# Kernel optimization log

Measured on AMD Instinct MI355X. Metric: run time of the kernel, lower is better.

The kernel has to match this reference:

```python
import jax, jax.numpy as jnp
import numpy as np

N, E, D = 20000, 320000, 256
EPS = 1e-5


def setup_inputs() -> dict:
    key = jax.random.key(0)
    ks = jax.random.split(key, 12)
    s = 1.0 / np.sqrt(D)
    s2 = 1.0 / np.sqrt(2 * D)
    return {
        "node_embeddings": jax.random.normal(ks[0], (N, D), jnp.float32),
        "edge_index": jax.random.randint(ks[1], (2, E), 0, N, jnp.int64),
        "edge_embeddings": jax.random.normal(ks[2], (E, D), jnp.float32),
        # message MLP: Linear(D,D) -> GELU -> Linear(D,D)
        "W1m": jax.random.uniform(ks[3], (D, D), jnp.float32, -s, s),
        "b1m": jnp.zeros((D,), jnp.float32),
        "W2m": jax.random.uniform(ks[4], (D, D), jnp.float32, -s, s),
        "b2m": jnp.zeros((D,), jnp.float32),
        # update MLP: Linear(D,2D) -> GELU -> Linear(2D,D)
        "W1u": jax.random.uniform(ks[5], (D, 2 * D), jnp.float32, -s, s),
        "b1u": jnp.zeros((2 * D,), jnp.float32),
        "W2u": jax.random.uniform(ks[6], (2 * D, D), jnp.float32, -s2, s2),
        "b2u": jnp.zeros((D,), jnp.float32),
        # LayerNorm params
        "gamma": jnp.ones((D,), jnp.float32),
        "beta": jnp.zeros((D,), jnp.float32),
    }


def _layer_norm(x, gamma, beta):
    mu = jnp.mean(x, axis=-1, keepdims=True)
    var = jnp.mean(jnp.square(x - mu), axis=-1, keepdims=True)
    return (x - mu) * jax.lax.rsqrt(var + EPS) * gamma + beta


def reference(node_embeddings, edge_index, edge_embeddings,
              W1m, b1m, W2m, b2m, W1u, b1u, W2u, b2u, gamma, beta):
    src = edge_index[0]
    dst = edge_index[1]
    n = node_embeddings.shape[0]
    # gather + edge add + message MLP (exact erf GELU, as torch default)
    h = node_embeddings[src] + edge_embeddings           # [E, D]
    h = jax.nn.gelu(h @ W1m + b1m, approximate=False)
    messages = h @ W2m + b2m                             # [E, D]
    # scatter-mean aggregation
    agg = jax.ops.segment_sum(messages, dst, num_segments=n)  # [N, D]
    deg = jax.ops.segment_sum(jnp.ones((dst.shape[0], 1), node_embeddings.dtype),
                              dst, num_segments=n)            # [N, 1]
    agg = agg / jnp.maximum(deg, 1.0)
    # update MLP + residual + LayerNorm
    u = jax.nn.gelu(agg @ W1u + b1u, approximate=False) @ W2u + b2u
    return _layer_norm(node_embeddings + u, gamma, beta)
```

## Files before the change

kernel.cpp:

```cpp
#include <hip/hip_runtime.h>
#include <hip/hip_bf16.h>

#define N_NODES 20000
#define N_EDGES 320000
#define EBLK 64
#define NBLK 32

typedef __attribute__((ext_vector_type(8))) short short8;
typedef __attribute__((ext_vector_type(4))) float f32x4;

static __device__ __forceinline__ unsigned short f2bf(float f) {
  __hip_bfloat16 h = __float2bfloat16(f);
  union { __hip_bfloat16 h; unsigned short u; } cv; cv.h = h; return cv.u;
}

static __device__ __forceinline__ unsigned int pk2(float a, float b) {
  return (unsigned int)f2bf(a) | ((unsigned int)f2bf(b) << 16);
}

static __device__ __forceinline__ float gelu_f(float x) {
  float z = x * (2.3022082f + 0.1029432f * x * x);
  z = fminf(fmaxf(z, -30.0f), 30.0f);
  float t = exp2f(z);
  return x * t * __frcp_rn(1.0f + t);
}

#define SWZ(row, byteoff) ((byteoff) ^ (((row) & 7) << 4))
#define SWZU(b) ((b) ^ ((((b) >> 8) & 7) << 4))

__global__ void init_kernel(float4* __restrict__ S4, int4* __restrict__ cnt4,
                            const float* __restrict__ W1m, const float* __restrict__ W2m,
                            const float* __restrict__ W1u, const float* __restrict__ W2u,
                            unsigned short* __restrict__ P1m, unsigned short* __restrict__ P2m,
                            unsigned short* __restrict__ P1u, unsigned short* __restrict__ P2u) {
  const int b = blockIdx.x;
  if (b < 5000) {
    int idx = b * blockDim.x + threadIdx.x;
    S4[idx] = make_float4(0.f, 0.f, 0.f, 0.f);
    if (idx < N_NODES / 4) cnt4[idx] = make_int4(0, 0, 0, 0);
    return;
  }
  int idx = (b - 5000) * blockDim.x + threadIdx.x;
  const float* W; unsigned short* P; int K, Nc, local;
  if (idx < 65536)        { W = W1m; P = P1m; K = 256; Nc = 256; local = idx; }
  else if (idx < 131072)  { W = W2m; P = P2m; K = 256; Nc = 256; local = idx - 65536; }
  else if (idx < 262144)  { W = W1u; P = P1u; K = 256; Nc = 512; local = idx - 131072; }
  else                    { W = W2u; P = P2u; K = 512; Nc = 256; local = idx - 262144; }
  int frag = local >> 9, wi = local & 511;
  int l = wi >> 3, i = wi & 7;
  int kf = K >> 5;
  int cf = frag / kf, t = frag % kf;
  int k = t * 32 + (l >> 4) * 8 + i;
  int n = cf * 16 + (l & 15);
  P[local] = f2bf(W[(size_t)k * Nc + n]);
}

__global__ void hist_kernel(const int* __restrict__ dst, int* __restrict__ cnt) {
  int e = blockIdx.x * blockDim.x + threadIdx.x;
  atomicAdd(&cnt[dst[e]], 1);
}

__global__ __launch_bounds__(1024) void scan_kernel(const int* __restrict__ cnt,
                                                    int* __restrict__ rptr,
                                                    int* __restrict__ cur) {
  __shared__ int sums[1024];
  const int t = threadIdx.x;
  const int base = t * 20;
  int local[20];
  int s = 0;
#pragma unroll
  for (int i = 0; i < 20; ++i) {
    int idx = base + i;
    int v = (idx < N_NODES) ? cnt[idx] : 0;
    local[i] = s;
    s += v;
  }
  int v = s;
  sums[t] = v;
  for (int off = 1; off < 1024; off <<= 1) {
    __syncthreads();
    int o = (t >= off) ? sums[t - off] : 0;
    __syncthreads();
    v += o;
    sums[t] = v;
  }
  int excl = v - s;
#pragma unroll
  for (int i = 0; i < 20; ++i) {
    int idx = base + i;
    if (idx < N_NODES) { int p = excl + local[i]; rptr[idx] = p; cur[idx] = p; }
  }
  if (t == 1023) rptr[N_NODES] = v;
}

__global__ void scatter_kernel(const int* __restrict__ dst, int* __restrict__ cur,
                               int* __restrict__ perm) {
  int e = blockIdx.x * blockDim.x + threadIdx.x;
  int d = dst[e];
  int pos = atomicAdd(&cur[d], 1);
  perm[pos] = e;
}

__global__ __launch_bounds__(512, 8) void edge_kernel(
    const float* __restrict__ node, const float* __restrict__ eemb,
    const int* __restrict__ src, const int* __restrict__ dst,
    const int* __restrict__ perm,
    const unsigned short* __restrict__ P1m, const float* __restrict__ b1m,
    float* __restrict__ S) {
  __shared__ unsigned short tA[EBLK * 256];
  __shared__ int dstS[EBLK];
  const int tid = threadIdx.x;
  const int e0 = blockIdx.x * EBLK;
  {
    const int r = tid >> 3;
    const int cs = (tid & 7) * 32;
    const int e = perm[e0 + r];
    const int se = src[e];
    if ((tid & 7) == 0) dstS[r] = dst[e];
    const float* ep = eemb + (size_t)e * 256 + cs;
    const float* np = node + (size_t)se * 256 + cs;
#pragma unroll
    for (int i = 0; i < 4; ++i) {
      float4 a = *(const float4*)(ep + i * 8);
      float4 b = *(const float4*)(np + i * 8);
      float4 c = *(const float4*)(ep + i * 8 + 4);
      float4 d = *(const float4*)(np + i * 8 + 4);
      uint4 p;
      p.x = pk2(a.x + b.x, a.y + b.y);
      p.y = pk2(a.z + b.z, a.w + b.w);
      p.z = pk2(c.x + d.x, c.y + d.y);
      p.w = pk2(c.z + d.z, c.w + d.w);
      *(uint4*)((char*)tA + SWZ(r, r * 512 + (cs + i * 8) * 2)) = p;
    }
  }
  __syncthreads();

  const int w = tid >> 6, l = tid & 63;
  const int lr = l & 15, lh = l >> 4;
  f32x4 acc[4][2];
#pragma unroll
  for (int c = 0; c < 2; ++c) {
    float bb = b1m[w * 32 + c * 16 + lr];
#pragma unroll
    for (int r4 = 0; r4 < 4; ++r4) acc[r4][c] = f32x4{bb, bb, bb, bb};
  }
#pragma unroll
  for (int kt = 0; kt < 8; ++kt) {
    short8 af[4];
#pragma unroll
    for (int r4 = 0; r4 < 4; ++r4) {
      int row = r4 * 16 + lr;
      af[r4] = *(const short8*)((const char*)tA + SWZ(row, row * 512 + kt * 64 + lh * 16));
    }
#pragma unroll
    for (int c = 0; c < 2; ++c) {
      short8 bfr = *(const short8*)(P1m + (size_t)(((w * 2 + c) * 8 + kt) * 512 + l * 8));
#pragma unroll
      for (int r4 = 0; r4 < 4; ++r4)
        acc[r4][c] = __builtin_amdgcn_mfma_f32_16x16x32_bf16(af[r4], bfr, acc[r4][c], 0, 0, 0);
    }
  }

#pragma unroll
  for (int r4 = 0; r4 < 4; ++r4)
#pragma unroll
    for (int c = 0; c < 2; ++c)
#pragma unroll
      for (int j = 0; j < 4; ++j)
        acc[r4][c][j] = gelu_f(acc[r4][c][j]);

  const int dv = dstS[l];
  const int pv = __shfl(dv, (l - 1) & 63);
  const bool bflag = (l == 0) || (dv != pv);
  const unsigned long long mask = __ballot(bflag);
  const int nseg = __popcll(mask);
  int sid[4][4];
#pragma unroll
  for (int r4 = 0; r4 < 4; ++r4)
#pragma unroll
    for (int j = 0; j < 4; ++j) {
      int row = r4 * 16 + lh * 4 + j;
      sid[r4][j] = __popcll(mask & ((2ULL << row) - 1)) - 1;
    }
  unsigned long long rem = mask;
  for (int s = 0; s < nseg; ++s) {
    const int rowf = __builtin_ctzll(rem);
    rem &= rem - 1;
    const int dseg = __shfl(dv, rowf);
    float p0 = 0.f, p1 = 0.f;
#pragma unroll
    for (int r4 = 0; r4 < 4; ++r4)
#pragma unroll
      for (int j = 0; j < 4; ++j) {
        bool m = (sid[r4][j] == s);
        p0 += m ? acc[r4][0][j] : 0.f;
        p1 += m ? acc[r4][1][j] : 0.f;
      }
    p0 += __shfl_xor(p0, 16); p0 += __shfl_xor(p0, 32);
    p1 += __shfl_xor(p1, 16); p1 += __shfl_xor(p1, 32);
    if (lh == 0) {
      float* Sp = S + (size_t)dseg * 256 + w * 32 + lr;
      atomicAdd(Sp, p0);
      atomicAdd(Sp + 16, p1);
    }
  }
}

__global__ __launch_bounds__(256, 4) void node_kernel(
    const float* __restrict__ node, const float* __restrict__ S, const int* __restrict__ rptr,
    const unsigned short* __restrict__ P2m, const float* __restrict__ b2m,
    const unsigned short* __restrict__ P1u, const float* __restrict__ b1u,
    const unsigned short* __restrict__ P2u, const float* __restrict__ b2u,
    const float* __restrict__ gamma, const float* __restrict__ beta,
    float* __restrict__ out) {
  __shared__ unsigned short tAB[2][NBLK * 256];
  __shared__ unsigned short tH[NBLK * 256];
  __shared__ float fmu[NBLK], frs[NBLK], fflag[NBLK];
  float* tU = (float*)tAB;
  const int tid = threadIdx.x;
  const int n0 = blockIdx.x * NBLK;
  const int r = tid >> 3;
  const int cs = (tid & 7) * 32;
  const int n = n0 + r;
  {
    int dgi = rptr[n + 1] - rptr[n];
    float rec = 1.0f / fmaxf((float)dgi, 1.0f);
    if ((tid & 7) == 0) fflag[r] = (dgi > 0) ? 1.0f : 0.0f;
    const float* sp = S + (size_t)n * 256 + cs;
#pragma unroll
    for (int i = 0; i < 4; ++i) {
      float4 a = *(const float4*)(sp + i * 8);
      float4 b = *(const float4*)(sp + i * 8 + 4);
      uint4 p;
      p.x = pk2(a.x * rec, a.y * rec);
      p.y = pk2(a.z * rec, a.w * rec);
      p.z = pk2(b.x * rec, b.y * rec);
      p.w = pk2(b.z * rec, b.w * rec);
      *(uint4*)((char*)tAB[0] + SWZ(r, r * 512 + (cs + i * 8) * 2)) = p;
    }
  }
  __syncthreads();
  const int w = tid >> 6, l = tid & 63, lr = l & 15, lh = l >> 4;

  {
    f32x4 acc[2][4];
#pragma unroll
    for (int r4 = 0; r4 < 2; ++r4)
#pragma unroll
      for (int c = 0; c < 4; ++c) acc[r4][c] = f32x4{0.f, 0.f, 0.f, 0.f};
#pragma unroll
    for (int t = 0; t < 8; ++t) {
      const int row0 = lr, row1 = 16 + lr;
      short8 af0 = *(const short8*)((const char*)tAB[0] + SWZ(row0, row0 * 512 + t * 64 + lh * 16));
      short8 af1 = *(const short8*)((const char*)tAB[0] + SWZ(row1, row1 * 512 + t * 64 + lh * 16));
#pragma unroll
      for (int c = 0; c < 4; ++c) {
        short8 bfr = *(const short8*)(P2m + (size_t)(((w * 4 + c) * 8 + t) * 512 + l * 8));
        acc[0][c] = __builtin_amdgcn_mfma_f32_16x16x32_bf16(af0, bfr, acc[0][c], 0, 0, 0);
        acc[1][c] = __builtin_amdgcn_mfma_f32_16x16x32_bf16(af1, bfr, acc[1][c], 0, 0, 0);
      }
    }
#pragma unroll
    for (int r4 = 0; r4 < 2; ++r4)
#pragma unroll
      for (int c = 0; c < 4; ++c) {
        int col = w * 64 + c * 16 + lr;
        float bm = b2m[col];
#pragma unroll
        for (int j = 0; j < 4; ++j) {
          int row = r4 * 16 + lh * 4 + j;
          float v = acc[r4][c][j] + fflag[row] * bm;
          *(unsigned short*)((char*)tAB[1] + SWZ(row, row * 512 + col * 2)) = f2bf(v);
        }
      }
  }
  __syncthreads();

  f32x4 acc3[2][4];
#pragma unroll
  for (int c = 0; c < 4; ++c) {
    float bb = b2u[w * 64 + c * 16 + lr];
    acc3[0][c] = f32x4{bb, bb, bb, bb};
    acc3[1][c] = f32x4{bb, bb, bb, bb};
  }
#pragma unroll
  for (int half = 0; half < 2; ++half) {
    {
      f32x4 acc[2][4];
#pragma unroll
      for (int r4 = 0; r4 < 2; ++r4)
#pragma unroll
        for (int c = 0; c < 4; ++c) acc[r4][c] = f32x4{0.f, 0.f, 0.f, 0.f};
#pragma unroll
      for (int t = 0; t < 8; ++t) {
        const int row0 = lr, row1 = 16 + lr;
        short8 af0 = *(const short8*)((const char*)tAB[1] + SWZ(row0, row0 * 512 + t * 64 + lh * 16));
        short8 af1 = *(const short8*)((const char*)tAB[1] + SWZ(row1, row1 * 512 + t * 64 + lh * 16));
#pragma unroll
        for (int c = 0; c < 4; ++c) {
          short8 bfr = *(const short8*)(P1u + (size_t)(((half * 16 + w * 4 + c) * 8 + t) * 512 + l * 8));
          acc[0][c] = __builtin_amdgcn_mfma_f32_16x16x32_bf16(af0, bfr, acc[0][c], 0, 0, 0);
          acc[1][c] = __builtin_amdgcn_mfma_f32_16x16x32_bf16(af1, bfr, acc[1][c], 0, 0, 0);
        }
      }
#pragma unroll
      for (int r4 = 0; r4 < 2; ++r4)
#pragma unroll
        for (int c = 0; c < 4; ++c) {
          int col = w * 64 + c * 16 + lr;
          float b1 = b1u[half * 256 + col];
#pragma unroll
          for (int j = 0; j < 4; ++j) {
            int row = r4 * 16 + lh * 4 + j;
            float v = gelu_f(acc[r4][c][j] + b1);
            *(unsigned short*)((char*)tH + SWZ(row, row * 512 + col * 2)) = f2bf(v);
          }
        }
    }
    __syncthreads();
    {
#pragma unroll
      for (int tt = 0; tt < 8; ++tt) {
        const int row0 = lr, row1 = 16 + lr;
        short8 af0 = *(const short8*)((const char*)tH + SWZ(row0, row0 * 512 + tt * 64 + lh * 16));
        short8 af1 = *(const short8*)((const char*)tH + SWZ(row1, row1 * 512 + tt * 64 + lh * 16));
#pragma unroll
        for (int c = 0; c < 4; ++c) {
          short8 bfr = *(const short8*)(P2u + (size_t)(((w * 4 + c) * 16 + half * 8 + tt) * 512 + l * 8));
          acc3[0][c] = __builtin_amdgcn_mfma_f32_16x16x32_bf16(af0, bfr, acc3[0][c], 0, 0, 0);
          acc3[1][c] = __builtin_amdgcn_mfma_f32_16x16x32_bf16(af1, bfr, acc3[1][c], 0, 0, 0);
        }
      }
    }
    __syncthreads();
  }

#pragma unroll
  for (int r4 = 0; r4 < 2; ++r4)
#pragma unroll
    for (int c = 0; c < 4; ++c) {
      int col = w * 64 + c * 16 + lr;
#pragma unroll
      for (int j = 0; j < 4; ++j) {
        int row = r4 * 16 + lh * 4 + j;
        *(float*)((char*)tU + SWZU(row * 1024 + col * 4)) = acc3[r4][c][j];
      }
    }
  __syncthreads();

  {
    float sum = 0.f, sq = 0.f;
#pragma unroll
    for (int i = 0; i < 8; ++i) {
      int byte = SWZU(r * 1024 + (cs + i * 4) * 4);
      float4 v = *(float4*)((char*)tU + byte);
      const float4 nb = *(const float4*)(node + (size_t)n * 256 + cs + i * 4);
      v.x += nb.x; v.y += nb.y; v.z += nb.z; v.w += nb.w;
      *(float4*)((char*)tU + byte) = v;
      sum += v.x + v.y + v.z + v.w;
      sq += v.x * v.x + v.y * v.y + v.z * v.z + v.w * v.w;
    }
    sum += __shfl_xor(sum, 1); sum += __shfl_xor(sum, 2); sum += __shfl_xor(sum, 4);
    sq  += __shfl_xor(sq, 1);  sq  += __shfl_xor(sq, 2);  sq  += __shfl_xor(sq, 4);
    if ((tid & 7) == 0) {
      float mu = sum * (1.0f / 256.0f);
      fmu[r] = mu;
      frs[r] = rsqrtf(fmaxf(sq * (1.0f / 256.0f) - mu * mu, 0.0f) + 1e-5f);
    }
  }
  __syncthreads();
#pragma unroll
  for (int i = 0; i < 8; ++i) {
    int f4 = i * 256 + tid;
    int row = f4 >> 6;
    int c4 = f4 & 63;
    float4 v = *(float4*)((char*)tU + SWZU(row * 1024 + c4 * 16));
    float mu = fmu[row], rs = frs[row];
    float4 g  = *(const float4*)(gamma + c4 * 4);
    float4 bt = *(const float4*)(beta + c4 * 4);
    float4 o;
    o.x = (v.x - mu) * rs * g.x + bt.x;
    o.y = (v.y - mu) * rs * g.y + bt.y;
    o.z = (v.z - mu) * rs * g.z + bt.z;
    o.w = (v.w - mu) * rs * g.w + bt.w;
    *(float4*)(out + (size_t)(n0 + row) * 256 + c4 * 4) = o;
  }
}

extern "C" void kernel_launch(void* const* d_in, const int* in_sizes, int n_in,
                              void* d_out, int out_size, void* d_ws, size_t ws_size,
                              hipStream_t stream) {
  const float* node = (const float*)d_in[0];
  const int* eidx = (const int*)d_in[1];
  const float* eemb = (const float*)d_in[2];
  const float* W1m = (const float*)d_in[3];
  const float* b1m = (const float*)d_in[4];
  const float* W2m = (const float*)d_in[5];
  const float* b2m = (const float*)d_in[6];
  const float* W1u = (const float*)d_in[7];
  const float* b1u = (const float*)d_in[8];
  const float* W2u = (const float*)d_in[9];
  const float* b2u = (const float*)d_in[10];
  const float* gamma = (const float*)d_in[11];
  const float* beta = (const float*)d_in[12];
  float* out = (float*)d_out;

  char* ws = (char*)d_ws;
  int* cnt  = (int*)ws;
  int* rptr = (int*)(ws + 81920);
  int* cur  = (int*)(ws + 163840);
  int* perm = (int*)(ws + 245760);
  unsigned short* P1m = (unsigned short*)(ws + 1525760);
  unsigned short* P2m = (unsigned short*)(ws + 1656832);
  unsigned short* P1u = (unsigned short*)(ws + 1787904);
  unsigned short* P2u = (unsigned short*)(ws + 2050048);
  const int* src = eidx;
  const int* dst = eidx + N_EDGES;

  init_kernel<<<5000 + 1536, 256, 0, stream>>>((float4*)out, (int4*)cnt,
                                               W1m, W2m, W1u, W2u, P1m, P2m, P1u, P2u);
  hist_kernel<<<N_EDGES / 256, 256, 0, stream>>>(dst, cnt);
  scan_kernel<<<1, 1024, 0, stream>>>(cnt, rptr, cur);
  scatter_kernel<<<N_EDGES / 256, 256, 0, stream>>>(dst, cur, perm);
  edge_kernel<<<N_EDGES / EBLK, 512, 0, stream>>>(node, eemb, src, dst, perm, P1m, b1m, out);
  node_kernel<<<N_NODES / NBLK, 256, 0, stream>>>(node, out, rptr, P2m, b2m,
                                                  P1u, b1u, P2u, b2u, gamma, beta, out);
}
```

Baseline: 348.6 us.

## Precompute node@W1m per node and aggregate segments via shared-memory slots

Uses linearity to split (node[src]+edge)@W1m into a per-node product computed once by a new nw1_kernel and stored as bf16, plus the per-edge product. The edge kernel no longer gathers 256 fp32 node values per edge; it reads two bf16 values per output element from the precomputed table instead. Segment reduction now accumulates into 16 shared-memory slots with LDS atomics, and interior segments are stored directly instead of using global atomics. This adds an extra kernel launch and extra bf16 rounding on the node term, and lowers the edge kernel's occupancy hint.

New measurement: 696.3 us. 2x slower.

```diff
diff --git a/kernel.cpp b/kernel.cpp
--- a/kernel.cpp
+++ b/kernel.cpp
@@ -5,6 +5,7 @@
 #define N_EDGES 320000
 #define EBLK 64
 #define NBLK 32
+#define NSLOT 16
 
 typedef __attribute__((ext_vector_type(8))) short short8;
 typedef __attribute__((ext_vector_type(4))) float f32x4;
@@ -12,6 +13,10 @@
 static __device__ __forceinline__ unsigned short f2bf(float f) {
   __hip_bfloat16 h = __float2bfloat16(f);
   union { __hip_bfloat16 h; unsigned short u; } cv; cv.h = h; return cv.u;
+}
+
+static __device__ __forceinline__ float bf2f(unsigned short u) {
+  union { unsigned int u; float f; } cv; cv.u = ((unsigned int)u) << 16; return cv.f;
 }
 
 static __device__ __forceinline__ unsigned int pk2(float a, float b) {
@@ -101,35 +106,85 @@
   perm[pos] = e;
 }
 
-__global__ __launch_bounds__(512, 8) void edge_kernel(
-    const float* __restrict__ node, const float* __restrict__ eemb,
+__global__ __launch_bounds__(256, 4) void nw1_kernel(
+    const float* __restrict__ node, const unsigned short* __restrict__ P1m,
+    const float* __restrict__ b1m, unsigned short* __restrict__ NW1) {
+  __shared__ unsigned short tA[NBLK * 256];
+  const int tid = threadIdx.x;
+  const int n0 = blockIdx.x * NBLK;
+  {
+    const int r = tid >> 3;
+    const int cs = (tid & 7) * 32;
+    const float* np = node + (size_t)(n0 + r) * 256 + cs;
+#pragma unroll
+    for (int i = 0; i < 4; ++i) {
+      float4 a = *(const float4*)(np + i * 8);
+      float4 b = *(const float4*)(np + i * 8 + 4);
+      uint4 p;
+      p.x = pk2(a.x, a.y); p.y = pk2(a.z, a.w);
+      p.z = pk2(b.x, b.y); p.w = pk2(b.z, b.w);
+      *(uint4*)((char*)tA + SWZ(r, r * 512 + (cs + i * 8) * 2)) = p;
+    }
+  }
+  __syncthreads();
+  const int w = tid >> 6, l = tid & 63, lr = l & 15, lh = l >> 4;
+  f32x4 acc[2][4];
+#pragma unroll
+  for (int r4 = 0; r4 < 2; ++r4)
+#pragma unroll
+    for (int c = 0; c < 4; ++c) acc[r4][c] = f32x4{0.f, 0.f, 0.f, 0.f};
+#pragma unroll
+  for (int t = 0; t < 8; ++t) {
+    const int row0 = lr, row1 = 16 + lr;
+    short8 af0 = *(const short8*)((const char*)tA + SWZ(row0, row0 * 512 + t * 64 + lh * 16));
+    short8 af1 = *(const short8*)((const char*)tA + SWZ(row1, row1 * 512 + t * 64 + lh * 16));
+#pragma unroll
+    for (int c = 0; c < 4; ++c) {
+      short8 bfr = *(const short8*)(P1m + (size_t)(((w * 4 + c) * 8 + t) * 512 + l * 8));
+      acc[0][c] = __builtin_amdgcn_mfma_f32_16x16x32_bf16(af0, bfr, acc[0][c], 0, 0, 0);
+      acc[1][c] = __builtin_amdgcn_mfma_f32_16x16x32_bf16(af1, bfr, acc[1][c], 0, 0, 0);
+    }
+  }
+#pragma unroll
+  for (int r4 = 0; r4 < 2; ++r4)
+#pragma unroll
+    for (int c = 0; c < 4; ++c) {
+      int col = w * 64 + c * 16 + lr;
+      float bb = b1m[col];
+#pragma unroll
+      for (int j = 0; j < 4; ++j) {
+        int row = r4 * 16 + lh * 4 + j;
+        NW1[(size_t)(n0 + row) * 256 + col] = f2bf(acc[r4][c][j] + bb);
+      }
+    }
+}
+
+__global__ __launch_bounds__(512, 6) void edge_kernel(
+    const float* __restrict__ eemb,
     const int* __restrict__ src, const int* __restrict__ dst,
     const int* __restrict__ perm,
-    const unsigned short* __restrict__ P1m, const float* __restrict__ b1m,
+    const unsigned short* __restrict__ P1m, const unsigned short* __restrict__ NW1,
     float* __restrict__ S) {
   __shared__ unsigned short tA[EBLK * 256];
-  __shared__ int dstS[EBLK];
+  __shared__ float slots[NSLOT * 256];
+  __shared__ int dstS[EBLK], srcS[EBLK], dsegL[NSLOT];
   const int tid = threadIdx.x;
   const int e0 = blockIdx.x * EBLK;
   {
     const int r = tid >> 3;
     const int cs = (tid & 7) * 32;
     const int e = perm[e0 + r];
-    const int se = src[e];
-    if ((tid & 7) == 0) dstS[r] = dst[e];
+    if ((tid & 7) == 0) { dstS[r] = dst[e]; srcS[r] = src[e]; }
+    *(float4*)(slots + tid * 8) = make_float4(0.f, 0.f, 0.f, 0.f);
+    *(float4*)(slots + tid * 8 + 4) = make_float4(0.f, 0.f, 0.f, 0.f);
     const float* ep = eemb + (size_t)e * 256 + cs;
-    const float* np = node + (size_t)se * 256 + cs;
 #pragma unroll
     for (int i = 0; i < 4; ++i) {
       float4 a = *(const float4*)(ep + i * 8);
-      float4 b = *(const float4*)(np + i * 8);
-      float4 c = *(const float4*)(ep + i * 8 + 4);
-      float4 d = *(const float4*)(np + i * 8 + 4);
+      float4 b = *(const float4*)(ep + i * 8 + 4);
       uint4 p;
-      p.x = pk2(a.x + b.x, a.y + b.y);
-      p.y = pk2(a.z + b.z, a.w + b.w);
-      p.z = pk2(c.x + d.x, c.y + d.y);
-      p.w = pk2(c.z + d.z, c.w + d.w);
+      p.x = pk2(a.x, a.y); p.y = pk2(a.z, a.w);
+      p.z = pk2(b.x, b.y); p.w = pk2(b.z, b.w);
       *(uint4*)((char*)tA + SWZ(r, r * 512 + (cs + i * 8) * 2)) = p;
     }
   }
@@ -139,11 +194,9 @@
   const int lr = l & 15, lh = l >> 4;
   f32x4 acc[4][2];
 #pragma unroll
-  for (int c = 0; c < 2; ++c) {
-    float bb = b1m[w * 32 + c * 16 + lr];
-#pragma unroll
-    for (int r4 = 0; r4 < 4; ++r4) acc[r4][c] = f32x4{bb, bb, bb, bb};
-  }
+  for (int r4 = 0; r4 < 4; ++r4)
+#pragma unroll
+    for (int c = 0; c < 2; ++c) acc[r4][c] = f32x4{0.f, 0.f, 0.f, 0.f};
 #pragma unroll
   for (int kt = 0; kt < 8; ++kt) {
     short8 af[4];
@@ -161,47 +214,83 @@
     }
   }
 
+  const int colbase = w * 32 + lr;
 #pragma unroll
   for (int r4 = 0; r4 < 4; ++r4)
 #pragma unroll
-    for (int c = 0; c < 2; ++c)
-#pragma unroll
-      for (int j = 0; j < 4; ++j)
-        acc[r4][c][j] = gelu_f(acc[r4][c][j]);
+    for (int j = 0; j < 4; ++j) {
+      int row = r4 * 16 + lh * 4 + j;
+      const unsigned short* nwp = NW1 + (size_t)srcS[row] * 256 + colbase;
+      float n0v = bf2f(nwp[0]);
+      float n1v = bf2f(nwp[16]);
+      acc[r4][0][j] = gelu_f(acc[r4][0][j] + n0v);
+      acc[r4][1][j] = gelu_f(acc[r4][1][j] + n1v);
+    }
 
   const int dv = dstS[l];
   const int pv = __shfl(dv, (l - 1) & 63);
   const bool bflag = (l == 0) || (dv != pv);
   const unsigned long long mask = __ballot(bflag);
   const int nseg = __popcll(mask);
-  int sid[4][4];
-#pragma unroll
-  for (int r4 = 0; r4 < 4; ++r4)
-#pragma unroll
-    for (int j = 0; j < 4; ++j) {
-      int row = r4 * 16 + lh * 4 + j;
-      sid[r4][j] = __popcll(mask & ((2ULL << row) - 1)) - 1;
-    }
-  unsigned long long rem = mask;
-  for (int s = 0; s < nseg; ++s) {
-    const int rowf = __builtin_ctzll(rem);
-    rem &= rem - 1;
-    const int dseg = __shfl(dv, rowf);
-    float p0 = 0.f, p1 = 0.f;
+
+  if (nseg <= NSLOT) {
+    if (w == 0 && bflag) {
+      int s = __popcll(mask & ((2ULL << l) - 1)) - 1;
+      dsegL[s] = dv;
+    }
 #pragma unroll
     for (int r4 = 0; r4 < 4; ++r4)
 #pragma unroll
       for (int j = 0; j < 4; ++j) {
-        bool m = (sid[r4][j] == s);
-        p0 += m ? acc[r4][0][j] : 0.f;
-        p1 += m ? acc[r4][1][j] : 0.f;
-      }
-    p0 += __shfl_xor(p0, 16); p0 += __shfl_xor(p0, 32);
-    p1 += __shfl_xor(p1, 16); p1 += __shfl_xor(p1, 32);
-    if (lh == 0) {
-      float* Sp = S + (size_t)dseg * 256 + w * 32 + lr;
-      atomicAdd(Sp, p0);
-      atomicAdd(Sp + 16, p1);
+        int row = r4 * 16 + lh * 4 + j;
+        int sid = __popcll(mask & ((2ULL << row) - 1)) - 1;
+        float* sp = slots + sid * 256 + colbase;
+        atomicAdd(sp, acc[r4][0][j]);
+        atomicAdd(sp + 16, acc[r4][1][j]);
+      }
+    __syncthreads();
+#pragma unroll
+    for (int t = 0; t < (NSLOT * 256) / 512; ++t) {
+      int idx = t * 512 + tid;
+      int s = idx >> 8;
+      int col = idx & 255;
+      if (s < nseg) {
+        float v = slots[idx];
+        float* gp = S + (size_t)dsegL[s] * 256 + col;
+        if (s == 0 || s == nseg - 1) atomicAdd(gp, v);
+        else *gp = v;
+      }
+    }
+  } else {
+    int sid[4][4];
+#pragma unroll
+    for (int r4 = 0; r4 < 4; ++r4)
+#pragma unroll
+      for (int j = 0; j < 4; ++j) {
+        int row = r4 * 16 + lh * 4 + j;
+        sid[r4][j] = __popcll(mask & ((2ULL << row) - 1)) - 1;
+      }
+    unsigned long long rem = mask;
+    for (int s = 0; s < nseg; ++s) {
+      const int rowf = __builtin_ctzll(rem);
+      rem &= rem - 1;
+      const int dseg = __shfl(dv, rowf);
+      float p0 = 0.f, p1 = 0.f;
+#pragma unroll
+      for (int r4 = 0; r4 < 4; ++r4)
+#pragma unroll
+        for (int j = 0; j < 4; ++j) {
+          bool m = (sid[r4][j] == s);
+          p0 += m ? acc[r4][0][j] : 0.f;
+          p1 += m ? acc[r4][1][j] : 0.f;
+        }
+      p0 += __shfl_xor(p0, 16); p0 += __shfl_xor(p0, 32);
+      p1 += __shfl_xor(p1, 16); p1 += __shfl_xor(p1, 32);
+      if (lh == 0) {
+        float* Sp = S + (size_t)dseg * 256 + w * 32 + lr;
+        atomicAdd(Sp, p0);
+        atomicAdd(Sp + 16, p1);
+      }
     }
   }
 }
@@ -414,6 +503,7 @@
   unsigned short* P2m = (unsigned short*)(ws + 1656832);
   unsigned short* P1u = (unsigned short*)(ws + 1787904);
   unsigned short* P2u = (unsigned short*)(ws + 2050048);
+  unsigned short* NW1 = (unsigned short*)(ws + 2312192);
   const int* src = eidx;
   const int* dst = eidx + N_EDGES;
 
@@ -422,7 +512,8 @@
   hist_kernel<<<N_EDGES / 256, 256, 0, stream>>>(dst, cnt);
   scan_kernel<<<1, 1024, 0, stream>>>(cnt, rptr, cur);
   scatter_kernel<<<N_EDGES / 256, 256, 0, stream>>>(dst, cur, perm);
-  edge_kernel<<<N_EDGES / EBLK, 512, 0, stream>>>(node, eemb, src, dst, perm, P1m, b1m, out);
+  nw1_kernel<<<N_NODES / NBLK, 256, 0, stream>>>(node, P1m, b1m, NW1);
+  edge_kernel<<<N_EDGES / EBLK, 512, 0, stream>>>(eemb, src, dst, perm, P1m, NW1, out);
   node_kernel<<<N_NODES / NBLK, 256, 0, stream>>>(node, out, rptr, P2m, b2m,
                                                   P1u, b1u, P2u, b2u, gamma, beta, out);
 }
```
